# Kernel tuning notes

Measured on AMD Instinct MI355X. Metric: run time of the kernel, lower is better.

The kernel has to match this reference:

```python
import jax, jax.numpy as jnp
import numpy as np

B, N, K, NUM_CLASSES = 8, 4096, 16, 40
M = B * N


def _safe_norm(v):
    s = jnp.sum(v * v, axis=-1)
    return jnp.where(s > 0, jnp.sqrt(jnp.where(s > 0, s, 1.0)), 0.0)


def _angle(v1, v2):
    cn = _safe_norm(jnp.cross(v1, v2))
    d = jnp.sum(v1 * v2, axis=-1)
    ok = (cn > 0) | (d != 0)
    return jnp.where(ok, jnp.arctan2(cn, jnp.where(ok, d, 1.0)), 0.0)


def _ppf(pos_i, pos_j, n_i, n_j):
    # PyG point_pair_features: pseudo = pos_j - pos_i (j = source, i = target)
    pseudo = pos_j - pos_i
    return jnp.stack([_safe_norm(pseudo), _angle(n_i, pseudo),
                      _angle(n_j, pseudo), _angle(n_i, n_j)], axis=-1)


def _knn_edges(pos):
    # knn_graph(k=K, loop=False), per-graph; returns (src, dst) with self-loops
    # appended (PPFConv add_self_loops=True default).
    p = pos.reshape(B, N, 3)
    sq = jnp.sum(p * p, axis=-1)                                   # [B,N]
    d2 = sq[:, :, None] + sq[:, None, :] - 2.0 * jnp.einsum('bnd,bmd->bnm', p, p)
    d2 = jnp.where(jnp.eye(N, dtype=bool)[None], jnp.inf, d2)      # no loops
    _, nbr = jax.lax.top_k(-d2, K)                                  # [B,N,K]
    offs = (jnp.arange(B) * N)[:, None, None]
    src = (nbr + offs).reshape(-1)                                  # neighbors j
    dst = jnp.repeat(jnp.arange(M), K)                              # targets i
    loops = jnp.arange(M)
    return jnp.concatenate([src, loops]), jnp.concatenate([dst, loops])


def _mlp(e, w1, b1, w2, b2):
    return jax.nn.relu(e @ w1 + b1) @ w2 + b2


def setup_inputs() -> dict:
    key = jax.random.key(0)
    ks = jax.random.split(key, 12)
    pos = jax.random.normal(ks[0], (M, 3), jnp.float32)
    nrm = jax.random.normal(ks[1], (M, 3), jnp.float32)
    nrm = nrm / jnp.linalg.norm(nrm, axis=-1, keepdims=True)
    batch = jnp.repeat(jnp.arange(B, dtype=jnp.int32), N)
    s = 0.1
    return {
        'pos': pos, 'normal': nrm, 'batch': batch,
        'w1a': jax.random.normal(ks[2], (4, 32)) * s,  'b1a': jnp.zeros(32),
        'w1b': jax.random.normal(ks[3], (32, 32)) * s, 'b1b': jnp.zeros(32),
        'w2a': jax.random.normal(ks[4], (36, 32)) * s, 'b2a': jnp.zeros(32),
        'w2b': jax.random.normal(ks[5], (32, 32)) * s, 'b2b': jnp.zeros(32),
        'wc':  jax.random.normal(ks[6], (32, NUM_CLASSES)) * s,
        'bc':  jnp.zeros(NUM_CLASSES),
    }


def reference(pos, normal, batch, w1a, b1a, w1b, b1b, w2a, b2a, w2b, b2b, wc, bc):
    src, dst = _knn_edges(pos)
    feats = _ppf(pos[dst], pos[src], normal[dst], normal[src])      # [E,4]
    # conv1: x=None -> message = mlp1(ppf), scatter-max per target node
    msg1 = _mlp(feats, w1a, b1a, w1b, b1b)
    x = jax.nn.relu(jax.ops.segment_max(msg1, dst, num_segments=M))  # [M,32]
    # conv2: message = mlp2([x_j, ppf])
    msg2 = _mlp(jnp.concatenate([x[src], feats], axis=-1), w2a, b2a, w2b, b2b)
    x = jax.nn.relu(jax.ops.segment_max(msg2, dst, num_segments=M))
    # global_max_pool over each graph (uniform batch: reshape)
    g = x.reshape(B, N, 32).max(axis=1)                              # [B,32]
    return g @ wc + bc                                               # [B,40]
```

## Files before the change

kernel.cpp:

```cpp
#include <hip/hip_runtime.h>
#include <hip/hip_bf16.h>
#include <math.h>

#define NB 8
#define NN 4096
#define KK 16
#define MM (NB*NN)
#define CH 32
#define SLOTS 17
#define NCLS 40
#define BIG 3.0e38f
#define CAP 96
#define NBLK2 (MM/8)

#define OW1A 0
#define OB1A 128
#define OW1B 160
#define OB1B 1184
#define OW2A 1216
#define OB2A 2368
#define OW2B 2400
#define OB2B 3424
#define OWC  3456
#define OBC  4736
#define NWTS 4776

__device__ float4 g_pos4[MM];
__device__ float4 g_nrm4[MM];
__device__ int    g_nbr[MM*KK];
__device__ float  g_u[MM*CH];
__device__ float  g_bmax[NBLK2*CH];
__device__ float  g_wts[NWTS];
__device__ int    g_isf32;

__device__ __forceinline__ float bf(const __hip_bfloat16 x) { return __bfloat162float(x); }

__device__ __forceinline__ float ldf(const void* p, int i, bool f32) {
  return f32 ? ((const float*)p)[i] : bf(((const __hip_bfloat16*)p)[i]);
}

__device__ __forceinline__ float angf(float ax, float ay, float az,
                                      float bx, float by, float bz) {
  float cx = ay*bz - az*by;
  float cy = az*bx - ax*bz;
  float cz = ax*by - ay*bx;
  float s  = cx*cx + cy*cy + cz*cz;
  float cn = s > 0.f ? sqrtf(s) : 0.f;
  float d  = ax*bx + ay*by + az*bz;
  return (cn > 0.f || d != 0.f) ? atan2f(cn, d) : 0.f;
}

__device__ __forceinline__ void ppf4(const float4 pi, const float4 ni,
                                     const float4 pj, const float4 nj, float* f) {
  float px = pj.x - pi.x, py = pj.y - pi.y, pz = pj.z - pi.z;
  float s = px*px + py*py + pz*pz;
  f[0] = s > 0.f ? sqrtf(s) : 0.f;
  f[1] = angf(ni.x, ni.y, ni.z, px, py, pz);
  f[2] = angf(nj.x, nj.y, nj.z, px, py, pz);
  f[3] = angf(ni.x, ni.y, ni.z, nj.x, nj.y, nj.z);
}

__device__ __forceinline__ unsigned int fkey(float f) {
  unsigned int u = __float_as_uint(f);
  return (u & 0x80000000u) ? ~u : (u | 0x80000000u);
}
__device__ __forceinline__ float funkey(unsigned int k) {
  unsigned int u = (k & 0x80000000u) ? (k ^ 0x80000000u) : ~k;
  return __uint_as_float(u);
}

__global__ __launch_bounds__(256) void wprep_kernel(
    const void* nrm, const void* w1a, const void* b1a, const void* w1b,
    const void* b1b, const void* w2a, const void* b2a, const void* w2b,
    const void* b2b, const void* wc, const void* bc) {
  __shared__ int sflag;
  const int tid = threadIdx.x;
  if (tid < 64) {
    const float* nf = (const float*)nrm;
    const __hip_bfloat16* nh = (const __hip_bfloat16*)nrm;
    float x = nf[3*tid], y = nf[3*tid+1], z = nf[3*tid+2];
    float ss = x*x + y*y + z*z;
    bool okf = (ss > 0.98f && ss < 1.02f);
    float a = bf(nh[3*tid]), b2 = bf(nh[3*tid+1]), c2 = bf(nh[3*tid+2]);
    float sb = a*a + b2*b2 + c2*c2;
    bool okb = (sb > 0.95f && sb < 1.05f);
    unsigned long long mf = __ballot(okf), mb = __ballot(okb);
    if (tid == 0) {
      sflag = (__popcll(mf) >= __popcll(mb)) ? 1 : 0;
      g_isf32 = sflag;
    }
  }
  __syncthreads();
  const bool f32 = sflag != 0;
  for (int i = tid; i < 128;  i += 256) g_wts[OW1A + i] = ldf(w1a, i, f32);
  for (int i = tid; i < 32;   i += 256) g_wts[OB1A + i] = ldf(b1a, i, f32);
  for (int i = tid; i < 1024; i += 256) g_wts[OW1B + i] = ldf(w1b, i, f32);
  for (int i = tid; i < 32;   i += 256) g_wts[OB1B + i] = ldf(b1b, i, f32);
  for (int i = tid; i < 1152; i += 256) g_wts[OW2A + i] = ldf(w2a, i, f32);
  for (int i = tid; i < 32;   i += 256) g_wts[OB2A + i] = ldf(b2a, i, f32);
  for (int i = tid; i < 1024; i += 256) g_wts[OW2B + i] = ldf(w2b, i, f32);
  for (int i = tid; i < 32;   i += 256) g_wts[OB2B + i] = ldf(b2b, i, f32);
  for (int i = tid; i < 1280; i += 256) g_wts[OWC  + i] = ldf(wc,  i, f32);
  for (int i = tid; i < 40;   i += 256) g_wts[OBC  + i] = ldf(bc,  i, f32);
}

__global__ __launch_bounds__(256) void prep_kernel(const void* __restrict__ pos,
                                                   const void* __restrict__ nrm) {
  const bool f32 = g_isf32 != 0;
  int i = blockIdx.x*256 + threadIdx.x;
  float x = ldf(pos, 3*i, f32), y = ldf(pos, 3*i+1, f32), z = ldf(pos, 3*i+2, f32);
  float sq = x*x + y*y + z*z;
  g_pos4[i] = make_float4(x, y, z, sq);
  float a = ldf(nrm, 3*i, f32), b = ldf(nrm, 3*i+1, f32), c = ldf(nrm, 3*i+2, f32);
  g_nrm4[i] = make_float4(a, b, c, 0.f);
}

__global__ __launch_bounds__(512) void knn_kernel() {
  __shared__ float sx[NN], sy[NN], sz[NN];
  __shared__ unsigned short ilst[64][CAP];
  __shared__ double dlst[8][CAP];
  __shared__ int    cnt[64];
  const int tid  = threadIdx.x;
  const int w    = tid >> 6, lane = tid & 63;
  const int blk  = blockIdx.x;
  const int b    = blk >> 6;
  const int qbw  = ((blk & 63) << 6) | (w << 3);
  const float4* bp = g_pos4 + b*NN;

  #pragma unroll
  for (int k = 0; k < 8; ++k) {
    int idx = k*512 + tid;
    float4 o = bp[idx];
    sx[idx] = o.x; sy[idx] = o.y; sz[idx] = o.z;
  }
  __syncthreads();

  float q2x[8], q2y[8], q2z[8];
  #pragma unroll
  for (int qq = 0; qq < 8; ++qq) {
    int qi = qbw + qq;
    q2x[qq] = -2.f*sx[qi]; q2y[qq] = -2.f*sy[qi]; q2z[qq] = -2.f*sz[qi];
  }

  float mn[8];
  #pragma unroll
  for (int qq = 0; qq < 8; ++qq) mn[qq] = BIG;
  #pragma unroll 4
  for (int it = 0; it < 64; ++it) {
    int idx = it*64 + lane;
    float ox = sx[idx], oy = sy[idx], oz = sz[idx];
    float ow = __builtin_fmaf(oz, oz, __builtin_fmaf(oy, oy, ox*ox));
    #pragma unroll
    for (int qq = 0; qq < 8; ++qq) {
      float d = __builtin_fmaf(q2x[qq], ox,
                __builtin_fmaf(q2y[qq], oy,
                __builtin_fmaf(q2z[qq], oz, ow)));
      mn[qq] = fminf(mn[qq], d);
    }
  }

  unsigned int key[8], lo[8], hi[8];
  #pragma unroll
  for (int qq = 0; qq < 8; ++qq) { key[qq] = fkey(mn[qq]); lo[qq] = 0u; hi[qq] = 0xFFFFFFFFu; }
  #pragma unroll 1
  for (int s = 0; s < 32; ++s) {
    #pragma unroll
    for (int qq = 0; qq < 8; ++qq) {
      unsigned int mid = lo[qq] + ((hi[qq] - lo[qq]) >> 1);
      int c = (int)__popcll(__ballot(key[qq] <= mid));
      if (c >= 17) hi[qq] = mid; else lo[qq] = mid + 1;
    }
  }
  float Tf[8];
  #pragma unroll
  for (int qq = 0; qq < 8; ++qq) {
    float T = funkey(hi[qq]);
    Tf[qq] = T + 4e-5f + 1e-5f*fabsf(T);
  }

  if (lane < 8) cnt[(w<<3) | lane] = 0;

  #pragma unroll 4
  for (int it = 0; it < 64; ++it) {
    int idx = it*64 + lane;
    float ox = sx[idx], oy = sy[idx], oz = sz[idx];
    float ow = __builtin_fmaf(oz, oz, __builtin_fmaf(oy, oy, ox*ox));
    #pragma unroll
    for (int qq = 0; qq < 8; ++qq) {
      float d = __builtin_fmaf(q2x[qq], ox,
                __builtin_fmaf(q2y[qq], oy,
                __builtin_fmaf(q2z[qq], oz, ow)));
      if (d <= Tf[qq] && idx != qbw + qq) {
        int p = atomicAdd(&cnt[(w<<3)|qq], 1);
        if (p < CAP) ilst[(w<<3)|qq][p] = (unsigned short)idx;
      }
    }
  }

  #pragma unroll 1
  for (int qq = 0; qq < 8; ++qq) {
    const int qi = qbw + qq;
    const int m = min(cnt[(w<<3)|qq], CAP);
    const double mx = (double)sx[qi], my_ = (double)sy[qi], mz = (double)sz[qi];
    const double sqme = (mx*mx + my_*my_) + mz*mz;
    for (int e = lane; e < m; e += 64) {
      int ci = ilst[(w<<3)|qq][e];
      double ox = (double)sx[ci], oy = (double)sy[ci], oz = (double)sz[ci];
      double sqo = (ox*ox + oy*oy) + oz*oz;
      double dt  = (mx*ox + my_*oy) + mz*oz;
      dlst[w][e] = (sqme + sqo) - 2.0*dt;
    }
    for (int e = lane; e < m; e += 64) {
      double myd = dlst[w][e];
      int myi = ilst[(w<<3)|qq][e];
      int rank = 0;
      for (int o = 0; o < m; ++o) {
        double od = dlst[w][o];
        int oi = ilst[(w<<3)|qq][o];
        rank += (od < myd) || (od == myd && oi < myi);
      }
      if (rank < KK) g_nbr[(b*NN + qi)*KK + rank] = b*NN + myi;
    }
  }
}

__global__ __launch_bounds__(256) void conv1_kernel() {
  __shared__ __align__(16) float fe[136][4];
  __shared__ __align__(16) float h1s[8*SLOTS*CH];
  __shared__ __align__(16) float xs[8][CH];
  const int tid = threadIdx.x;
  const int c = tid & 31;
  const int node0 = blockIdx.x << 3;
  float w1a_c[4], w1b_c[32], w2a_c[32];
  #pragma unroll
  for (int f = 0; f < 4; ++f)  w1a_c[f] = g_wts[OW1A + f*CH + c];
  #pragma unroll
  for (int k = 0; k < 32; ++k) w1b_c[k] = g_wts[OW1B + k*CH + c];
  #pragma unroll
  for (int k = 0; k < 32; ++k) w2a_c[k] = g_wts[OW2A + k*CH + c];
  const float b1a_c = g_wts[OB1A + c], b1b_c = g_wts[OB1B + c];

  if (tid < 136) {
    int ns = tid / 17, slot = tid - ns*17;
    int i = node0 + ns;
    int j = (slot < KK) ? g_nbr[i*KK + slot] : i;
    ppf4(g_pos4[i], g_nrm4[i], g_pos4[j], g_nrm4[j], fe[tid]);
  }
  __syncthreads();
  #pragma unroll
  for (int it = 0; it < 17; ++it) {
    int idx = it*256 + tid;
    int e = idx >> 5;
    float4 f4 = *(const float4*)fe[e];
    float h = b1a_c + f4.x*w1a_c[0] + f4.y*w1a_c[1] + f4.z*w1a_c[2] + f4.w*w1a_c[3];
    h1s[idx] = fmaxf(h, 0.f);
  }
  __syncthreads();
  const int ns = tid >> 5;
  const int i  = node0 + ns;
  float acc = -BIG;
  #pragma unroll
  for (int slot = 0; slot < SLOTS; ++slot) {
    const float* hr = &h1s[(ns*SLOTS + slot)*CH];
    float msg = b1b_c;
    #pragma unroll
    for (int k4 = 0; k4 < 8; ++k4) {
      float4 h4 = *(const float4*)(hr + 4*k4);
      msg += h4.x*w1b_c[4*k4] + h4.y*w1b_c[4*k4+1] + h4.z*w1b_c[4*k4+2] + h4.w*w1b_c[4*k4+3];
    }
    acc = fmaxf(acc, msg);
  }
  xs[ns][c] = fmaxf(acc, 0.f);
  __syncthreads();
  float uu = 0.f;
  #pragma unroll
  for (int k4 = 0; k4 < 8; ++k4) {
    float4 x4 = *(const float4*)&xs[ns][4*k4];
    uu += x4.x*w2a_c[4*k4] + x4.y*w2a_c[4*k4+1] + x4.z*w2a_c[4*k4+2] + x4.w*w2a_c[4*k4+3];
  }
  g_u[i*CH + c] = uu;
}

__global__ __launch_bounds__(256) void conv2_kernel() {
  __shared__ __align__(16) float fe[136][4];
  __shared__ int jn[136];
  __shared__ __align__(16) float h2s[8*SLOTS*CH];
  __shared__ float xs[8][CH];
  const int tid = threadIdx.x;
  const int c = tid & 31;
  const int node0 = blockIdx.x << 3;
  float w2aL_c[4], w2b_c[32];
  #pragma unroll
  for (int f = 0; f < 4; ++f)  w2aL_c[f] = g_wts[OW2A + (CH + f)*CH + c];
  #pragma unroll
  for (int k = 0; k < 32; ++k) w2b_c[k] = g_wts[OW2B + k*CH + c];
  const float b2a_c = g_wts[OB2A + c], b2b_c = g_wts[OB2B + c];

  if (tid < 136) {
    int ns = tid / 17, slot = tid - ns*17;
    int i = node0 + ns;
    int j = (slot < KK) ? g_nbr[i*KK + slot] : i;
    jn[tid] = j;
    ppf4(g_pos4[i], g_nrm4[i], g_pos4[j], g_nrm4[j], fe[tid]);
  }
  __syncthreads();
  #pragma unroll
  for (int it = 0; it < 17; ++it) {
    int idx = it*256 + tid;
    int e = idx >> 5;
    float4 f4 = *(const float4*)fe[e];
    float uv = g_u[jn[e]*CH + c];
    float h = b2a_c + uv + f4.x*w2aL_c[0] + f4.y*w2aL_c[1] + f4.z*w2aL_c[2] + f4.w*w2aL_c[3];
    h2s[idx] = fmaxf(h, 0.f);
  }
  __syncthreads();
  const int ns = tid >> 5;
  float acc = -BIG;
  #pragma unroll
  for (int slot = 0; slot < SLOTS; ++slot) {
    const float* hr = &h2s[(ns*SLOTS + slot)*CH];
    float msg = b2b_c;
    #pragma unroll
    for (int k4 = 0; k4 < 8; ++k4) {
      float4 h4 = *(const float4*)(hr + 4*k4);
      msg += h4.x*w2b_c[4*k4] + h4.y*w2b_c[4*k4+1] + h4.z*w2b_c[4*k4+2] + h4.w*w2b_c[4*k4+3];
    }
    acc = fmaxf(acc, msg);
  }
  xs[ns][c] = fmaxf(acc, 0.f);
  __syncthreads();
  if (tid < CH) {
    float m2 = xs[0][c];
    #pragma unroll
    for (int r = 1; r < 8; ++r) m2 = fmaxf(m2, xs[r][c]);
    g_bmax[blockIdx.x*CH + c] = m2;
  }
}

__global__ __launch_bounds__(256) void head_kernel(float* __restrict__ out) {
  __shared__ float red[8][CH];
  __shared__ float gm[CH];
  const int g = blockIdx.x;
  const int c = threadIdx.x & 31, sub = threadIdx.x >> 5;
  const float* base = g_bmax + (size_t)(g*512 + sub*64)*CH;
  float mx = 0.f;
  #pragma unroll
  for (int n = 0; n < 64; ++n) mx = fmaxf(mx, base[n*CH + c]);
  red[sub][c] = mx;
  __syncthreads();
  if (threadIdx.x < CH) {
    float m2 = red[0][c];
    #pragma unroll
    for (int r = 1; r < 8; ++r) m2 = fmaxf(m2, red[r][c]);
    gm[c] = m2;
  }
  __syncthreads();
  if (threadIdx.x < NCLS) {
    int co = threadIdx.x;
    float s = g_wts[OBC + co];
    #pragma unroll
    for (int f = 0; f < CH; ++f) s += gm[f] * g_wts[OWC + f*NCLS + co];
    out[g*NCLS + co] = s;
  }
}

extern "C" void kernel_launch(void* const* d_in, const int* in_sizes, int n_in,
                              void* d_out, int out_size, void* d_ws, size_t ws_size,
                              hipStream_t stream) {
  const void* pos = d_in[0];
  const void* nrm = d_in[1];
  const void* w1a = d_in[3];
  const void* b1a = d_in[4];
  const void* w1b = d_in[5];
  const void* b1b = d_in[6];
  const void* w2a = d_in[7];
  const void* b2a = d_in[8];
  const void* w2b = d_in[9];
  const void* b2b = d_in[10];
  const void* wc  = d_in[11];
  const void* bc  = d_in[12];

  wprep_kernel<<<1,      256, 0, stream>>>(nrm, w1a, b1a, w1b, b1b, w2a, b2a, w2b, b2b, wc, bc);
  prep_kernel <<<MM/256, 256, 0, stream>>>(pos, nrm);
  knn_kernel  <<<MM/64,  512, 0, stream>>>();
  conv1_kernel<<<MM/8,   256, 0, stream>>>();
  conv2_kernel<<<MM/8,   256, 0, stream>>>();
  head_kernel <<<NB,     256, 0, stream>>>((float*)d_out);
}
```

Before: 228.3 us.

## Run second MLP layer of both convs on MFMA with split-bf16 precision

Replaces the per-thread scalar FP32 32x32 second-layer matmul in conv1 and conv2 with MFMA 16x16x32 bf16 instructions. Activations and weights are split into hi/lo bf16 pairs (three-product compensation) to keep close to fp32 accuracy, with pre-fragmented weights built in wprep. Edge rows are padded to 32 per node and stored in LDS with a padded stride, and the per-node max is reduced across lanes with shuffles. This trades VALU FMA work for matrix-core work plus extra split and conversion cost, and the split-bf16 scheme introduces some precision risk.

```diff
diff --git a/kernel.cpp b/kernel.cpp
--- a/kernel.cpp
+++ b/kernel.cpp
@@ -12,6 +12,7 @@
 #define BIG 3.0e38f
 #define CAP 96
 #define NBLK2 (MM/8)
+#define AROW 40
 
 #define OW1A 0
 #define OB1A 128
@@ -25,12 +26,17 @@
 #define OBC  4736
 #define NWTS 4776
 
+typedef short short8 __attribute__((ext_vector_type(8)));
+typedef float f32x4  __attribute__((ext_vector_type(4)));
+
 __device__ float4 g_pos4[MM];
 __device__ float4 g_nrm4[MM];
 __device__ int    g_nbr[MM*KK];
 __device__ float  g_u[MM*CH];
 __device__ float  g_bmax[NBLK2*CH];
 __device__ float  g_wts[NWTS];
+__device__ __align__(16) unsigned short g_wfrag1[2][2][64][8];
+__device__ __align__(16) unsigned short g_wfrag2[2][2][64][8];
 __device__ int    g_isf32;
 
 __device__ __forceinline__ float bf(const __hip_bfloat16 x) { return __bfloat162float(x); }
@@ -67,6 +73,14 @@
 __device__ __forceinline__ float funkey(unsigned int k) {
   unsigned int u = (k & 0x80000000u) ? (k ^ 0x80000000u) : ~k;
   return __uint_as_float(u);
+}
+
+__device__ __forceinline__ void bsplit(float v, unsigned short* hi, unsigned short* lo) {
+  __hip_bfloat16 h = __float2bfloat16(v);
+  float hf = __bfloat162float(h);
+  __hip_bfloat16 l = __float2bfloat16(v - hf);
+  *hi = *reinterpret_cast<unsigned short*>(&h);
+  *lo = *reinterpret_cast<unsigned short*>(&l);
 }
 
 __global__ __launch_bounds__(256) void wprep_kernel(
@@ -102,6 +116,22 @@
   for (int i = tid; i < 32;   i += 256) g_wts[OB2B + i] = ldf(b2b, i, f32);
   for (int i = tid; i < 1280; i += 256) g_wts[OWC  + i] = ldf(wc,  i, f32);
   for (int i = tid; i < 40;   i += 256) g_wts[OBC  + i] = ldf(bc,  i, f32);
+  for (int i = tid; i < 4096; i += 256) {
+    int which = i >> 11;
+    int r = i & 2047;
+    int t  = r >> 10;  r &= 1023;
+    int hl = r >> 9;   r &= 511;
+    int ln = r >> 3;
+    int j  = r & 7;
+    int k = (ln >> 4)*8 + j;
+    int c = t*16 + (ln & 15);
+    float wv = ldf(which ? w2b : w1b, k*CH + c, f32);
+    unsigned short hi, lo;
+    bsplit(wv, &hi, &lo);
+    unsigned short v = hl ? lo : hi;
+    if (which) g_wfrag2[t][hl][ln][j] = v;
+    else       g_wfrag1[t][hl][ln][j] = v;
+  }
 }
 
 __global__ __launch_bounds__(256) void prep_kernel(const void* __restrict__ pos,
@@ -226,19 +256,26 @@
 
 __global__ __launch_bounds__(256) void conv1_kernel() {
   __shared__ __align__(16) float fe[136][4];
-  __shared__ __align__(16) float h1s[8*SLOTS*CH];
+  __shared__ __align__(16) short aHi[256*AROW];
+  __shared__ __align__(16) short aLo[256*AROW];
   __shared__ __align__(16) float xs[8][CH];
   const int tid = threadIdx.x;
   const int c = tid & 31;
+  const int lane = tid & 63, wv = tid >> 6;
+  const int quad = lane >> 4, l15 = lane & 15;
   const int node0 = blockIdx.x << 3;
-  float w1a_c[4], w1b_c[32], w2a_c[32];
+  float w1a_c[4], w2a_c[32];
   #pragma unroll
   for (int f = 0; f < 4; ++f)  w1a_c[f] = g_wts[OW1A + f*CH + c];
   #pragma unroll
-  for (int k = 0; k < 32; ++k) w1b_c[k] = g_wts[OW1B + k*CH + c];
-  #pragma unroll
   for (int k = 0; k < 32; ++k) w2a_c[k] = g_wts[OW2A + k*CH + c];
-  const float b1a_c = g_wts[OB1A + c], b1b_c = g_wts[OB1B + c];
+  const float b1a_c = g_wts[OB1A + c];
+  short8 bH0 = *(const short8*)&g_wfrag1[0][0][lane][0];
+  short8 bL0 = *(const short8*)&g_wfrag1[0][1][lane][0];
+  short8 bH1 = *(const short8*)&g_wfrag1[1][0][lane][0];
+  short8 bL1 = *(const short8*)&g_wfrag1[1][1][lane][0];
+  const float bias0 = g_wts[OB1B + l15];
+  const float bias1 = g_wts[OB1B + 16 + l15];
 
   if (tid < 136) {
     int ns = tid / 17, slot = tid - ns*17;
@@ -251,50 +288,80 @@
   for (int it = 0; it < 17; ++it) {
     int idx = it*256 + tid;
     int e = idx >> 5;
+    int nd = e / 17, slot = e - nd*17;
     float4 f4 = *(const float4*)fe[e];
     float h = b1a_c + f4.x*w1a_c[0] + f4.y*w1a_c[1] + f4.z*w1a_c[2] + f4.w*w1a_c[3];
-    h1s[idx] = fmaxf(h, 0.f);
+    h = fmaxf(h, 0.f);
+    unsigned short hb, lb;
+    bsplit(h, &hb, &lb);
+    int row = nd*32 + slot;
+    aHi[row*AROW + c] = (short)hb;
+    aLo[row*AROW + c] = (short)lb;
+  }
+  __syncthreads();
+  #pragma unroll
+  for (int ni = 0; ni < 2; ++ni) {
+    const int n8 = wv*2 + ni;
+    const int rbase = n8*32;
+    short8 ah0 = *(const short8*)&aHi[(rbase      + l15)*AROW + quad*8];
+    short8 al0 = *(const short8*)&aLo[(rbase      + l15)*AROW + quad*8];
+    short8 ah1 = *(const short8*)&aHi[(rbase + 16 + l15)*AROW + quad*8];
+    short8 al1 = *(const short8*)&aLo[(rbase + 16 + l15)*AROW + quad*8];
+    f32x4 a00 = {0.f,0.f,0.f,0.f}, a01 = a00, a10 = a00, a11 = a00;
+    a00 = __builtin_amdgcn_mfma_f32_16x16x32_bf16(ah0, bH0, a00, 0, 0, 0);
+    a00 = __builtin_amdgcn_mfma_f32_16x16x32_bf16(ah0, bL0, a00, 0, 0, 0);
+    a00 = __builtin_amdgcn_mfma_f32_16x16x32_bf16(al0, bH0, a00, 0, 0, 0);
+    a01 = __builtin_amdgcn_mfma_f32_16x16x32_bf16(ah0, bH1, a01, 0, 0, 0);
+    a01 = __builtin_amdgcn_mfma_f32_16x16x32_bf16(ah0, bL1, a01, 0, 0, 0);
+    a01 = __builtin_amdgcn_mfma_f32_16x16x32_bf16(al0, bH1, a01, 0, 0, 0);
+    a10 = __builtin_amdgcn_mfma_f32_16x16x32_bf16(ah1, bH0, a10, 0, 0, 0);
+    a10 = __builtin_amdgcn_mfma_f32_16x16x32_bf16(ah1, bL0, a10, 0, 0, 0);
+    a10 = __builtin_amdgcn_mfma_f32_16x16x32_bf16(al1, bH0, a10, 0, 0, 0);
+    a11 = __builtin_amdgcn_mfma_f32_16x16x32_bf16(ah1, bH1, a11, 0, 0, 0);
+    a11 = __builtin_amdgcn_mfma_f32_16x16x32_bf16(ah1, bL1, a11, 0, 0, 0);
+    a11 = __builtin_amdgcn_mfma_f32_16x16x32_bf16(al1, bH1, a11, 0, 0, 0);
+    float m0 = fmaxf(fmaxf(a00[0], a00[1]), fmaxf(a00[2], a00[3]));
+    float m1 = fmaxf(fmaxf(a01[0], a01[1]), fmaxf(a01[2], a01[3]));
+    if (quad == 0) { m0 = fmaxf(m0, a10[0]); m1 = fmaxf(m1, a11[0]); }
+    m0 = fmaxf(m0, __shfl_xor(m0, 16)); m0 = fmaxf(m0, __shfl_xor(m0, 32));
+    m1 = fmaxf(m1, __shfl_xor(m1, 16)); m1 = fmaxf(m1, __shfl_xor(m1, 32));
+    if (quad == 0) {
+      xs[n8][l15]      = fmaxf(m0 + bias0, 0.f);
+      xs[n8][16 + l15] = fmaxf(m1 + bias1, 0.f);
+    }
   }
   __syncthreads();
   const int ns = tid >> 5;
-  const int i  = node0 + ns;
-  float acc = -BIG;
-  #pragma unroll
-  for (int slot = 0; slot < SLOTS; ++slot) {
-    const float* hr = &h1s[(ns*SLOTS + slot)*CH];
-    float msg = b1b_c;
-    #pragma unroll
-    for (int k4 = 0; k4 < 8; ++k4) {
-      float4 h4 = *(const float4*)(hr + 4*k4);
-      msg += h4.x*w1b_c[4*k4] + h4.y*w1b_c[4*k4+1] + h4.z*w1b_c[4*k4+2] + h4.w*w1b_c[4*k4+3];
-    }
-    acc = fmaxf(acc, msg);
-  }
-  xs[ns][c] = fmaxf(acc, 0.f);
-  __syncthreads();
   float uu = 0.f;
   #pragma unroll
   for (int k4 = 0; k4 < 8; ++k4) {
     float4 x4 = *(const float4*)&xs[ns][4*k4];
     uu += x4.x*w2a_c[4*k4] + x4.y*w2a_c[4*k4+1] + x4.z*w2a_c[4*k4+2] + x4.w*w2a_c[4*k4+3];
   }
-  g_u[i*CH + c] = uu;
+  g_u[(node0 + ns)*CH + c] = uu;
 }
 
 __global__ __launch_bounds__(256) void conv2_kernel() {
   __shared__ __align__(16) float fe[136][4];
   __shared__ int jn[136];
-  __shared__ __align__(16) float h2s[8*SLOTS*CH];
-  __shared__ float xs[8][CH];
+  __shared__ __align__(16) short aHi[256*AROW];
+  __shared__ __align__(16) short aLo[256*AROW];
+  __shared__ __align__(16) float xs[8][CH];
   const int tid = threadIdx.x;
   const int c = tid & 31;
+  const int lane = tid & 63, wv = tid >> 6;
+  const int quad = lane >> 4, l15 = lane & 15;
   const int node0 = blockIdx.x << 3;
-  float w2aL_c[4], w2b_c[32];
+  float w2aL_c[4];
   #pragma unroll
   for (int f = 0; f < 4; ++f)  w2aL_c[f] = g_wts[OW2A + (CH + f)*CH + c];
-  #pragma unroll
-  for (int k = 0; k < 32; ++k) w2b_c[k] = g_wts[OW2B + k*CH + c];
-  const float b2a_c = g_wts[OB2A + c], b2b_c = g_wts[OB2B + c];
+  const float b2a_c = g_wts[OB2A + c];
+  short8 bH0 = *(const short8*)&g_wfrag2[0][0][lane][0];
+  short8 bL0 = *(const short8*)&g_wfrag2[0][1][lane][0];
+  short8 bH1 = *(const short8*)&g_wfrag2[1][0][lane][0];
+  short8 bL1 = *(const short8*)&g_wfrag2[1][1][lane][0];
+  const float bias0 = g_wts[OB2B + l15];
+  const float bias1 = g_wts[OB2B + 16 + l15];
 
   if (tid < 136) {
     int ns = tid / 17, slot = tid - ns*17;
@@ -308,26 +375,49 @@
   for (int it = 0; it < 17; ++it) {
     int idx = it*256 + tid;
     int e = idx >> 5;
+    int nd = e / 17, slot = e - nd*17;
     float4 f4 = *(const float4*)fe[e];
     float uv = g_u[jn[e]*CH + c];
     float h = b2a_c + uv + f4.x*w2aL_c[0] + f4.y*w2aL_c[1] + f4.z*w2aL_c[2] + f4.w*w2aL_c[3];
-    h2s[idx] = fmaxf(h, 0.f);
-  }
-  __syncthreads();
-  const int ns = tid >> 5;
-  float acc = -BIG;
-  #pragma unroll
-  for (int slot = 0; slot < SLOTS; ++slot) {
-    const float* hr = &h2s[(ns*SLOTS + slot)*CH];
-    float msg = b2b_c;
-    #pragma unroll
-    for (int k4 = 0; k4 < 8; ++k4) {
-      float4 h4 = *(const float4*)(hr + 4*k4);
-      msg += h4.x*w2b_c[4*k4] + h4.y*w2b_c[4*k4+1] + h4.z*w2b_c[4*k4+2] + h4.w*w2b_c[4*k4+3];
-    }
-    acc = fmaxf(acc, msg);
-  }
-  xs[ns][c] = fmaxf(acc, 0.f);
+    h = fmaxf(h, 0.f);
+    unsigned short hb, lb;
+    bsplit(h, &hb, &lb);
+    int row = nd*32 + slot;
+    aHi[row*AROW + c] = (short)hb;
+    aLo[row*AROW + c] = (short)lb;
+  }
+  __syncthreads();
+  #pragma unroll
+  for (int ni = 0; ni < 2; ++ni) {
+    const int n8 = wv*2 + ni;
+    const int rbase = n8*32;
+    short8 ah0 = *(const short8*)&aHi[(rbase      + l15)*AROW + quad*8];
+    short8 al0 = *(const short8*)&aLo[(rbase      + l15)*AROW + quad*8];
+    short8 ah1 = *(const short8*)&aHi[(rbase + 16 + l15)*AROW + quad*8];
+    short8 al1 = *(const short8*)&aLo[(rbase + 16 + l15)*AROW + quad*8];
+    f32x4 a00 = {0.f,0.f,0.f,0.f}, a01 = a00, a10 = a00, a11 = a00;
+    a00 = __builtin_amdgcn_mfma_f32_16x16x32_bf16(ah0, bH0, a00, 0, 0, 0);
+    a00 = __builtin_amdgcn_mfma_f32_16x16x32_bf16(ah0, bL0, a00, 0, 0, 0);
+    a00 = __builtin_amdgcn_mfma_f32_16x16x32_bf16(al0, bH0, a00, 0, 0, 0);
+    a01 = __builtin_amdgcn_mfma_f32_16x16x32_bf16(ah0, bH1, a01, 0, 0, 0);
+    a01 = __builtin_amdgcn_mfma_f32_16x16x32_bf16(ah0, bL1, a01, 0, 0, 0);
+    a01 = __builtin_amdgcn_mfma_f32_16x16x32_bf16(al0, bH1, a01, 0, 0, 0);
+    a10 = __builtin_amdgcn_mfma_f32_16x16x32_bf16(ah1, bH0, a10, 0, 0, 0);
+    a10 = __builtin_amdgcn_mfma_f32_16x16x32_bf16(ah1, bL0, a10, 0, 0, 0);
+    a10 = __builtin_amdgcn_mfma_f32_16x16x32_bf16(al1, bH0, a10, 0, 0, 0);
+    a11 = __builtin_amdgcn_mfma_f32_16x16x32_bf16(ah1, bH1, a11, 0, 0, 0);
+    a11 = __builtin_amdgcn_mfma_f32_16x16x32_bf16(ah1, bL1, a11, 0, 0, 0);
+    a11 = __builtin_amdgcn_mfma_f32_16x16x32_bf16(al1, bH1, a11, 0, 0, 0);
+    float m0 = fmaxf(fmaxf(a00[0], a00[1]), fmaxf(a00[2], a00[3]));
+    float m1 = fmaxf(fmaxf(a01[0], a01[1]), fmaxf(a01[2], a01[3]));
+    if (quad == 0) { m0 = fmaxf(m0, a10[0]); m1 = fmaxf(m1, a11[0]); }
+    m0 = fmaxf(m0, __shfl_xor(m0, 16)); m0 = fmaxf(m0, __shfl_xor(m0, 32));
+    m1 = fmaxf(m1, __shfl_xor(m1, 16)); m1 = fmaxf(m1, __shfl_xor(m1, 32));
+    if (quad == 0) {
+      xs[n8][l15]      = fmaxf(m0 + bias0, 0.f);
+      xs[n8][16 + l15] = fmaxf(m1 + bias1, 0.f);
+    }
+  }
   __syncthreads();
   if (tid < CH) {
     float m2 = xs[0][c];
```

Result: no change. 227.0 us (-0.6%).
